# Optimization experiments

Hardware: AMD Instinct MI355X
Metric: run time of the kernel (lower is better)

Reference implementation:

```python
import jax, jax.numpy as jnp
import numpy as np

B, C, H, W = 4, 256, 64, 64
C8 = C // 8


def setup_inputs() -> dict:
    key = jax.random.key(0)
    k1, k2, k3, k4 = jax.random.split(key, 4)
    x = jax.random.normal(k1, (B, C, H, W), dtype=jnp.float32)
    # conv1d(ks=1, bias=False) projections -> plain [out, in] matrices
    Wq = jax.random.normal(k2, (C8, C), dtype=jnp.float32) * (1.0 / np.sqrt(C))
    Wk = jax.random.normal(k3, (C8, C), dtype=jnp.float32) * (1.0 / np.sqrt(C))
    Wv = jax.random.normal(k4, (C, C), dtype=jnp.float32) * (1.0 / np.sqrt(C))
    gamma = jnp.zeros((1,), dtype=jnp.float32)
    return {"x": x, "Wq": Wq, "Wk": Wk, "Wv": Wv, "gamma": gamma}


def reference(x, Wq, Wk, Wv, gamma):
    b, c, h, w = x.shape
    xf = x.reshape(b, c, h * w)                      # [B, C, N]
    f = jnp.einsum('oc,bcn->bon', Wq, xf)            # [B, C/8, N] query
    g = jnp.einsum('oc,bcn->bon', Wk, xf)            # [B, C/8, N] key
    hv = jnp.einsum('oc,bcn->bon', Wv, xf)           # [B, C,   N] value
    # scores[b,i,j] = sum_c f[b,c,i] * g[b,c,j]; softmax over dim=1 (i)
    scores = jnp.einsum('bci,bcj->bij', f, g)        # [B, N, N]
    beta = jax.nn.softmax(scores, axis=1)
    # o[b,c,j] = sum_i hv[b,c,i] * beta[b,i,j]
    o = jnp.einsum('bci,bij->bcj', hv, beta)         # [B, C, N]
    out = gamma[0] * o + xf
    return out.reshape(b, c, h, w)
```

## Files before the change

### kernel.cpp

```cpp
#include <hip/hip_runtime.h>

#define B_  4
#define C_  256
#define C8_ 32
#define N_  4096
#define HVS_ (N_ + 64)

#define TJ 128
#define KI 64
#define SPLITS 4

typedef __attribute__((ext_vector_type(8)))  short bf16x8;
typedef __attribute__((ext_vector_type(16))) float f32x16;

union FragAB { bf16x8 v; unsigned short u[8]; };

__device__ __forceinline__ unsigned short f2bf(float x) {
    unsigned u = __float_as_uint(x);
    unsigned r = u + 0x7FFFu + ((u >> 16) & 1u);
    return (unsigned short)(r >> 16);
}
__device__ __forceinline__ unsigned pack2bf(float a, float b) {
    return (unsigned)f2bf(a) | ((unsigned)f2bf(b) << 16);
}
__device__ __forceinline__ unsigned cvtpk(float lo, float hi) {
    unsigned r;
    asm("v_cvt_pk_bf16_f32 %0, %1, %2" : "=v"(r) : "v"(lo), "v"(hi));
    return r;
}

__global__ __launch_bounds__(256) void prep_w_kernel(
    const float* __restrict__ Wq, const float* __restrict__ Wk,
    const float* __restrict__ Wv, unsigned short* __restrict__ Wbf)
{
    int idx = (blockIdx.x * 256 + threadIdx.x) * 4;
    int row = idx >> 8;
    int col = idx & 255;
    const float* src; int r;
    if (row < 32)      { src = Wq; r = row;      }
    else if (row < 64) { src = Wk; r = row - 32; }
    else               { src = Wv; r = row - 64; }
    float4 v = *(const float4*)&src[r * 256 + col];
    uint2 o; o.x = pack2bf(v.x, v.y); o.y = pack2bf(v.z, v.w);
    *(uint2*)&Wbf[idx] = o;
}

__global__ __launch_bounds__(256) void proj_mfma_kernel(
    const float* __restrict__ x, const unsigned short* __restrict__ Wbf,
    unsigned short* __restrict__ fT, unsigned* __restrict__ gdw,
    unsigned short* __restrict__ hv)
{
    __shared__ unsigned short T[32][264];
    int t = threadIdx.x, w = t >> 6, lane = t & 63;
    int half = lane >> 5, l31 = lane & 31;
    int b  = blockIdx.y;
    int n0 = blockIdx.x * 32;

    {
        const float* xb = x + (size_t)b * C_ * N_;
        int cr = t >> 3;
        int nc = (t & 7) * 4;
#pragma unroll
        for (int p = 0; p < 8; ++p) {
            int c = p * 32 + cr;
            float4 v = *(const float4*)&xb[(size_t)c * N_ + n0 + nc];
            T[nc + 0][c] = f2bf(v.x);
            T[nc + 1][c] = f2bf(v.y);
            T[nc + 2][c] = f2bf(v.z);
            T[nc + 3][c] = f2bf(v.w);
        }
    }
    __syncthreads();

    int nm = (w < 2) ? 3 : 2;
    int mt0 = w, mt1 = w + 4, mt2 = w + 8;

    bf16x8 bfr[16];
#pragma unroll
    for (int ks = 0; ks < 16; ++ks)
        bfr[ks] = *(const bf16x8*)&T[l31][ks * 16 + half * 8];

    f32x16 acc[3];
#pragma unroll
    for (int a = 0; a < 3; ++a) acc[a] = (f32x16)0.f;

#pragma unroll
    for (int ks = 0; ks < 16; ++ks) {
        int kofs = ks * 16 + half * 8;
        bf16x8 a0 = *(const bf16x8*)&Wbf[(size_t)(mt0 * 32 + l31) * 256 + kofs];
        acc[0] = __builtin_amdgcn_mfma_f32_32x32x16_bf16(a0, bfr[ks], acc[0], 0, 0, 0);
        bf16x8 a1 = *(const bf16x8*)&Wbf[(size_t)(mt1 * 32 + l31) * 256 + kofs];
        acc[1] = __builtin_amdgcn_mfma_f32_32x32x16_bf16(a1, bfr[ks], acc[1], 0, 0, 0);
        if (nm == 3) {
            bf16x8 a2 = *(const bf16x8*)&Wbf[(size_t)(mt2 * 32 + l31) * 256 + kofs];
            acc[2] = __builtin_amdgcn_mfma_f32_32x32x16_bf16(a2, bfr[ks], acc[2], 0, 0, 0);
        }
    }

    unsigned short* fTb = fT  + (size_t)b * N_ * C8_;
    unsigned*       gb  = gdw + (size_t)b * (C8_ / 2) * N_;
    unsigned short* hb  = hv  + (size_t)b * C_ * HVS_;
#pragma unroll
    for (int im = 0; im < 3; ++im) {
        if (im >= nm) break;
        int mt = (im == 0) ? mt0 : (im == 1) ? mt1 : mt2;
        if (mt == 0) {
#pragma unroll
            for (int rp = 0; rp < 8; ++rp) {
                int r = 2 * rp;
                int R = (r & 3) + 8 * (r >> 2) + 4 * half;
                *(unsigned*)&fTb[(size_t)(n0 + l31) * C8_ + R] = cvtpk(acc[0][r], acc[0][r + 1]);
            }
        } else if (mt == 1) {
#pragma unroll
            for (int rp = 0; rp < 8; ++rp) {
                int r = 2 * rp;
                int R = (r & 3) + 8 * (r >> 2) + 4 * half;
                gb[(size_t)(R >> 1) * N_ + n0 + l31] = cvtpk(acc[1][r], acc[1][r + 1]);
            }
        } else {
#pragma unroll
            for (int rp = 0; rp < 8; ++rp) {
                int r = 2 * rp;
                int R = mt * 32 + (r & 3) + 8 * (r >> 2) + 4 * half - 64;
                unsigned u = cvtpk(acc[im][r], acc[im][r + 1]);
                hb[(size_t)R * HVS_ + n0 + l31]       = (unsigned short)(u & 0xffffu);
                hb[(size_t)(R + 1) * HVS_ + n0 + l31] = (unsigned short)(u >> 16);
            }
        }
    }
}

__global__ __launch_bounds__(256, 2) void flash_kernel(
    const unsigned short* __restrict__ fT, const unsigned* __restrict__ gdw,
    const unsigned short* __restrict__ hv, unsigned* __restrict__ o_part,
    float* __restrict__ l_part)
{
    __shared__ unsigned short fS[64][40];
    __shared__ unsigned short hvT[256][72];
    __shared__ unsigned short pT[128][72];

    int t    = threadIdx.x;
    int w    = t >> 6;
    int lane = t & 63;
    int half = lane >> 5;
    int l31  = lane & 31;

    int d  = blockIdx.x;
    int jb = (d >> 3) & 31;
    int p  = (d & 7) | (((d >> 8) & 1) << 3);
    int b  = p & 3;
    int s  = p >> 2;
    int j0 = jb * TJ;

    const unsigned short* fb = fT  + (size_t)b * N_ * C8_;
    const unsigned*       gb = gdw + (size_t)b * (C8_ / 2) * N_;
    const unsigned short* hb = hv  + (size_t)b * C_ * HVS_;

    FragAB gf[2];
#pragma unroll
    for (int ks = 0; ks < 2; ++ks)
#pragma unroll
        for (int q = 0; q < 4; ++q) {
            unsigned dv = gb[(size_t)(ks * 8 + half * 4 + q) * N_ + j0 + w * 32 + l31];
            gf[ks].u[2 * q]     = (unsigned short)(dv & 0xffffu);
            gf[ks].u[2 * q + 1] = (unsigned short)(dv >> 16);
        }

    f32x16 acc[8];
#pragma unroll
    for (int a = 0; a < 8; ++a) acc[a] = (f32x16)0.f;
    float lacc = 0.f;

    int i_begin = s * (N_ / SPLITS);
    int i_end   = i_begin + N_ / SPLITS;

    for (int i0 = i_begin; i0 < i_end; i0 += KI) {
        __syncthreads();

        {
            int il = t >> 2, c4 = (t & 3) * 8;
            *(uint4*)&fS[il][c4] = *(const uint4*)&fb[(size_t)(i0 + il) * C8_ + c4];
        }
        {
            int crow  = t >> 3;
            int chunk = t & 7;
#pragma unroll
            for (int q = 0; q < 8; ++q) {
                int c = crow + 32 * q;
                *(uint4*)&hvT[c][chunk * 8] =
                    *(const uint4*)&hb[(size_t)c * HVS_ + i0 + chunk * 8];
            }
        }
        __syncthreads();

#pragma unroll
        for (int it = 0; it < 2; ++it) {
            bf16x8 af0 = *(const bf16x8*)&fS[it * 32 + l31][half * 8];
            bf16x8 af1 = *(const bf16x8*)&fS[it * 32 + l31][16 + half * 8];
            f32x16 sacc = (f32x16)0.f;
            sacc = __builtin_amdgcn_mfma_f32_32x32x16_bf16(af0, gf[0].v, sacc, 0, 0, 0);
            sacc = __builtin_amdgcn_mfma_f32_32x32x16_bf16(af1, gf[1].v, sacc, 0, 0, 0);
            float pv[16];
#pragma unroll
            for (int r = 0; r < 16; ++r) pv[r] = __expf(sacc[r]);
            float s0 = (pv[0]  + pv[1])  + (pv[2]  + pv[3]);
            float s1 = (pv[4]  + pv[5])  + (pv[6]  + pv[7]);
            float s2 = (pv[8]  + pv[9])  + (pv[10] + pv[11]);
            float s3 = (pv[12] + pv[13]) + (pv[14] + pv[15]);
            lacc += (s0 + s1) + (s2 + s3);
            int jr = w * 32 + l31;
#pragma unroll
            for (int a = 0; a < 4; ++a) {
                uint2 u;
                u.x = cvtpk(pv[4 * a + 0], pv[4 * a + 1]);
                u.y = cvtpk(pv[4 * a + 2], pv[4 * a + 3]);
                *(uint2*)&pT[jr][it * 32 + 8 * a + 4 * half] = u;
            }
        }
        __syncthreads();

        __builtin_amdgcn_s_setprio(1);
#pragma unroll
        for (int ks4 = 0; ks4 < 4; ++ks4) {
            int kofs = ks4 * 16 + half * 8;
            bf16x8 af[2], bfr[4];
#pragma unroll
            for (int ct = 0; ct < 2; ++ct)
                af[ct] = *(const bf16x8*)&hvT[w * 64 + ct * 32 + l31][kofs];
#pragma unroll
            for (int jt = 0; jt < 4; ++jt)
                bfr[jt] = *(const bf16x8*)&pT[jt * 32 + l31][kofs];
#pragma unroll
            for (int ct = 0; ct < 2; ++ct)
#pragma unroll
                for (int jt = 0; jt < 4; ++jt)
                    acc[ct * 4 + jt] = __builtin_amdgcn_mfma_f32_32x32x16_bf16(
                        af[ct], bfr[jt], acc[ct * 4 + jt], 0, 0, 0);
        }
        __builtin_amdgcn_s_setprio(0);
    }

    unsigned* ob = o_part + (size_t)(b * SPLITS + s) * (C_ / 2) * N_;
#pragma unroll
    for (int ct = 0; ct < 2; ++ct)
#pragma unroll
        for (int jt = 0; jt < 4; ++jt) {
            f32x16 a = acc[ct * 4 + jt];
#pragma unroll
            for (int rp = 0; rp < 8; ++rp) {
                int r = 2 * rp;
                unsigned u = cvtpk(a[r], a[r + 1]);
                int c = w * 64 + ct * 32 + (r & 3) + 8 * (r >> 2) + 4 * half;
                ob[(size_t)(c >> 1) * N_ + j0 + jt * 32 + l31] = u;
            }
        }
    float lsum = lacc + __shfl_down(lacc, 32);
    if (lane < 32)
        l_part[(size_t)(b * SPLITS + s) * N_ + j0 + w * 32 + lane] = lsum;
}

__global__ __launch_bounds__(256) void combine_kernel(
    const unsigned* __restrict__ o_part, const float* __restrict__ l_part,
    const float* __restrict__ x, const float* __restrict__ gamma,
    float* __restrict__ out)
{
    int j = (blockIdx.x * 256 + threadIdx.x) * 4;
    int b = blockIdx.z;
    float4 l4 = {0.f, 0.f, 0.f, 0.f};
#pragma unroll
    for (int s = 0; s < SPLITS; ++s) {
        float4 lv = *(const float4*)&l_part[(size_t)(b * SPLITS + s) * N_ + j];
        l4.x += lv.x; l4.y += lv.y; l4.z += lv.z; l4.w += lv.w;
    }
    float4 inv = {1.f / l4.x, 1.f / l4.y, 1.f / l4.z, 1.f / l4.w};
    float gm = gamma[0];
#pragma unroll
    for (int cc = 0; cc < 2; ++cc) {
        int c2 = blockIdx.y * 2 + cc;
        float4 olo = {0.f, 0.f, 0.f, 0.f}, ohi = {0.f, 0.f, 0.f, 0.f};
#pragma unroll
        for (int s = 0; s < SPLITS; ++s) {
            uint4 u = *(const uint4*)&o_part[((size_t)(b * SPLITS + s) * (C_ / 2) + c2) * N_ + j];
            olo.x += __uint_as_float(u.x << 16); ohi.x += __uint_as_float(u.x & 0xffff0000u);
            olo.y += __uint_as_float(u.y << 16); ohi.y += __uint_as_float(u.y & 0xffff0000u);
            olo.z += __uint_as_float(u.z << 16); ohi.z += __uint_as_float(u.z & 0xffff0000u);
            olo.w += __uint_as_float(u.w << 16); ohi.w += __uint_as_float(u.w & 0xffff0000u);
        }
        size_t i0 = ((size_t)b * C_ + 2 * c2) * N_ + j;
        float4 x0 = *(const float4*)&x[i0];
        float4 x1 = *(const float4*)&x[i0 + N_];
        float4 r0 = {gm * olo.x * inv.x + x0.x, gm * olo.y * inv.y + x0.y,
                     gm * olo.z * inv.z + x0.z, gm * olo.w * inv.w + x0.w};
        float4 r1 = {gm * ohi.x * inv.x + x1.x, gm * ohi.y * inv.y + x1.y,
                     gm * ohi.z * inv.z + x1.z, gm * ohi.w * inv.w + x1.w};
        *(float4*)&out[i0] = r0;
        *(float4*)&out[i0 + N_] = r1;
    }
}

extern "C" void kernel_launch(void* const* d_in, const int* in_sizes, int n_in,
                              void* d_out, int out_size, void* d_ws, size_t ws_size,
                              hipStream_t stream) {
    const float* x     = (const float*)d_in[0];
    const float* Wq    = (const float*)d_in[1];
    const float* Wk    = (const float*)d_in[2];
    const float* Wv    = (const float*)d_in[3];
    const float* gamma = (const float*)d_in[4];
    float* out = (float*)d_out;

    char* ws = (char*)d_ws;
    unsigned* o_part = (unsigned*)ws;
    float* l_part = (float*)(o_part + (size_t)SPLITS * B_ * (C_ / 2) * N_);
    unsigned short* fT  = (unsigned short*)(l_part + (size_t)SPLITS * B_ * N_);
    unsigned*       gdw = (unsigned*)(fT + (size_t)B_ * N_ * C8_);
    unsigned short* hv  = (unsigned short*)(gdw + (size_t)B_ * (C8_ / 2) * N_);
    unsigned short* Wbf = hv  + (size_t)B_ * C_ * HVS_;

    prep_w_kernel<<<dim3(80), 256, 0, stream>>>(Wq, Wk, Wv, Wbf);

    proj_mfma_kernel<<<dim3(N_ / 32, B_), 256, 0, stream>>>(x, Wbf, fT, gdw, hv);

    flash_kernel<<<dim3((N_ / TJ) * B_ * SPLITS), 256, 0, stream>>>(fT, gdw, hv, o_part, l_part);

    combine_kernel<<<dim3(N_ / 1024, C_ / 4, B_), 256, 0, stream>>>(o_part, l_part, x, gamma, out);
}
```

Baseline: 139.5 us.

## Fuse split-combine into flash kernel via last-block atomic counter

Removes the separate combine kernel. Each flash block increments a per-(batch, column-tile) atomic counter after writing its partials, and the last of the split blocks reduces the partial outputs and row sums, applies gamma, and adds the residual. This saves one kernel launch and lets the combine overlap with other flash blocks. In exchange it adds thread fences and atomics, and the reduction runs in only a subset of blocks with scalar, less vectorized loads, which may create a tail at the end of the flash kernel.

```diff
diff --git a/kernel.cpp b/kernel.cpp
--- a/kernel.cpp
+++ b/kernel.cpp
@@ -48,13 +48,16 @@
 __global__ __launch_bounds__(256) void proj_mfma_kernel(
     const float* __restrict__ x, const unsigned short* __restrict__ Wbf,
     unsigned short* __restrict__ fT, unsigned* __restrict__ gdw,
-    unsigned short* __restrict__ hv)
+    unsigned short* __restrict__ hv, unsigned* __restrict__ counters)
 {
     __shared__ unsigned short T[32][264];
     int t = threadIdx.x, w = t >> 6, lane = t & 63;
     int half = lane >> 5, l31 = lane & 31;
     int b  = blockIdx.y;
     int n0 = blockIdx.x * 32;
+
+    if (blockIdx.x == 0 && blockIdx.y == 0 && t < B_ * 32)
+        counters[t] = 0;
 
     {
         const float* xb = x + (size_t)b * C_ * N_;
@@ -134,11 +137,14 @@
 __global__ __launch_bounds__(256, 2) void flash_kernel(
     const unsigned short* __restrict__ fT, const unsigned* __restrict__ gdw,
     const unsigned short* __restrict__ hv, unsigned* __restrict__ o_part,
-    float* __restrict__ l_part)
+    float* __restrict__ l_part, const float* __restrict__ x,
+    const float* __restrict__ gamma, float* __restrict__ out,
+    unsigned* __restrict__ counters)
 {
     __shared__ unsigned short fS[64][40];
     __shared__ unsigned short hvT[256][72];
     __shared__ unsigned short pT[128][72];
+    __shared__ unsigned oldc;
 
     int t    = threadIdx.x;
     int w    = t >> 6;
@@ -258,44 +264,36 @@
     float lsum = lacc + __shfl_down(lacc, 32);
     if (lane < 32)
         l_part[(size_t)(b * SPLITS + s) * N_ + j0 + w * 32 + lane] = lsum;
-}
-
-__global__ __launch_bounds__(256) void combine_kernel(
-    const unsigned* __restrict__ o_part, const float* __restrict__ l_part,
-    const float* __restrict__ x, const float* __restrict__ gamma,
-    float* __restrict__ out)
-{
-    int j = (blockIdx.x * 256 + threadIdx.x) * 4;
-    int b = blockIdx.z;
-    float4 l4 = {0.f, 0.f, 0.f, 0.f};
-#pragma unroll
-    for (int s = 0; s < SPLITS; ++s) {
-        float4 lv = *(const float4*)&l_part[(size_t)(b * SPLITS + s) * N_ + j];
-        l4.x += lv.x; l4.y += lv.y; l4.z += lv.z; l4.w += lv.w;
-    }
-    float4 inv = {1.f / l4.x, 1.f / l4.y, 1.f / l4.z, 1.f / l4.w};
-    float gm = gamma[0];
-#pragma unroll
-    for (int cc = 0; cc < 2; ++cc) {
-        int c2 = blockIdx.y * 2 + cc;
-        float4 olo = {0.f, 0.f, 0.f, 0.f}, ohi = {0.f, 0.f, 0.f, 0.f};
-#pragma unroll
-        for (int s = 0; s < SPLITS; ++s) {
-            uint4 u = *(const uint4*)&o_part[((size_t)(b * SPLITS + s) * (C_ / 2) + c2) * N_ + j];
-            olo.x += __uint_as_float(u.x << 16); ohi.x += __uint_as_float(u.x & 0xffff0000u);
-            olo.y += __uint_as_float(u.y << 16); ohi.y += __uint_as_float(u.y & 0xffff0000u);
-            olo.z += __uint_as_float(u.z << 16); ohi.z += __uint_as_float(u.z & 0xffff0000u);
-            olo.w += __uint_as_float(u.w << 16); ohi.w += __uint_as_float(u.w & 0xffff0000u);
-        }
-        size_t i0 = ((size_t)b * C_ + 2 * c2) * N_ + j;
-        float4 x0 = *(const float4*)&x[i0];
-        float4 x1 = *(const float4*)&x[i0 + N_];
-        float4 r0 = {gm * olo.x * inv.x + x0.x, gm * olo.y * inv.y + x0.y,
-                     gm * olo.z * inv.z + x0.z, gm * olo.w * inv.w + x0.w};
-        float4 r1 = {gm * ohi.x * inv.x + x1.x, gm * ohi.y * inv.y + x1.y,
-                     gm * ohi.z * inv.z + x1.z, gm * ohi.w * inv.w + x1.w};
-        *(float4*)&out[i0] = r0;
-        *(float4*)&out[i0 + N_] = r1;
+
+    __threadfence();
+    __syncthreads();
+    if (t == 0) oldc = atomicAdd(&counters[b * 32 + jb], 1);
+    __syncthreads();
+    if (oldc == SPLITS - 1) {
+        __threadfence();
+        if (t == 0) counters[b * 32 + jb] = 0;
+        float gm = gamma[0];
+        int jj = t & 127;
+        int j  = j0 + jj;
+        float l = 0.f;
+#pragma unroll
+        for (int ss = 0; ss < SPLITS; ++ss)
+            l += l_part[(size_t)(b * SPLITS + ss) * N_ + j];
+        float inv = 1.f / l;
+        int c2base = (t >> 7) * 64;
+        for (int cq = 0; cq < 64; ++cq) {
+            int c2 = c2base + cq;
+            float olo = 0.f, ohi = 0.f;
+#pragma unroll
+            for (int ss = 0; ss < SPLITS; ++ss) {
+                unsigned u = o_part[((size_t)(b * SPLITS + ss) * (C_ / 2) + c2) * N_ + j];
+                olo += __uint_as_float(u << 16);
+                ohi += __uint_as_float(u & 0xffff0000u);
+            }
+            size_t ix = ((size_t)b * C_ + 2 * c2) * N_ + j;
+            out[ix]      = gm * olo * inv + x[ix];
+            out[ix + N_] = gm * ohi * inv + x[ix + N_];
+        }
     }
 }
 
@@ -316,12 +314,12 @@
     unsigned*       gdw = (unsigned*)(fT + (size_t)B_ * N_ * C8_);
     unsigned short* hv  = (unsigned short*)(gdw + (size_t)B_ * (C8_ / 2) * N_);
     unsigned short* Wbf = hv  + (size_t)B_ * C_ * HVS_;
+    unsigned* counters  = (unsigned*)(Wbf + (size_t)(C_ + 2 * C8_) * C_);
 
     prep_w_kernel<<<dim3(80), 256, 0, stream>>>(Wq, Wk, Wv, Wbf);
 
-    proj_mfma_kernel<<<dim3(N_ / 32, B_), 256, 0, stream>>>(x, Wbf, fT, gdw, hv);
-
-    flash_kernel<<<dim3((N_ / TJ) * B_ * SPLITS), 256, 0, stream>>>(fT, gdw, hv, o_part, l_part);
-
-    combine_kernel<<<dim3(N_ / 1024, C_ / 4, B_), 256, 0, stream>>>(o_part, l_part, x, gamma, out);
-}
+    proj_mfma_kernel<<<dim3(N_ / 32, B_), 256, 0, stream>>>(x, Wbf, fT, gdw, hv, counters);
+
+    flash_kernel<<<dim3((N_ / TJ) * B_ * SPLITS), 256, 0, stream>>>(
+        fT, gdw, hv, o_part, l_part, x, gamma, out, counters);
+}
```

Measured after the change: 217.5 us. 1.56x slower.
